# Kernel tuning notes

Measured on AMD Instinct MI355X. Metric: run time of the kernel, lower is better.

## Reference

```python
import jax, jax.numpy as jnp
import numpy as np
from jax import lax

EPS = 1e-5

def ste_sign(x):
    # forward-only module: plain sign is fine
    return jnp.sign(x)

def conv2d(x, w, pad):
    # x: NCHW, w: OIHW, stride 1
    return lax.conv_general_dilated(x, w, window_strides=(1, 1),
                                    padding=[(pad, pad), (pad, pad)],
                                    dimension_numbers=('NCHW', 'OIHW', 'NCHW'))

def maxpool2(x):
    # 2x2 max pool, stride 2, VALID (floor) -- matches nn.MaxPool2d(2,2)
    return lax.reduce_window(x, -jnp.inf, lax.max, (1, 1, 2, 2), (1, 1, 2, 2), 'VALID')

def batchnorm(x, gamma, beta):
    # training-mode BN: batch statistics over (N,H,W), biased variance
    mean = jnp.mean(x, axis=(0, 2, 3), keepdims=True)
    var = jnp.var(x, axis=(0, 2, 3), keepdims=True)
    xn = (x - mean) * lax.rsqrt(var + EPS)
    return xn * gamma[None, :, None, None] + beta[None, :, None, None]

def setup_inputs() -> dict:
    key = jax.random.key(0)
    ks = jax.random.split(key, 8)
    def he(k, shape):
        n = shape[2] * shape[3] * shape[0]
        return jax.random.normal(k, shape, jnp.float32) * np.sqrt(2.0 / n)
    x = jax.random.normal(ks[0], (4096, 1, 28, 28), jnp.float32)
    w0 = he(ks[1], (32, 1, 3, 3))
    w1 = he(ks[2], (32, 32, 3, 3))
    w2 = he(ks[3], (32, 32, 3, 3))
    g0 = jnp.ones((32,), jnp.float32); b0 = jnp.zeros((32,), jnp.float32)
    g1 = jnp.ones((32,), jnp.float32); b1 = jnp.zeros((32,), jnp.float32)
    g2 = jnp.ones((32,), jnp.float32); b2 = jnp.zeros((32,), jnp.float32)
    fw = jax.random.normal(ks[4], (10, 288), jnp.float32) * 0.01
    fb = jnp.zeros((10,), jnp.float32)
    return {"x": x, "w0": w0, "g0": g0, "b0": b0, "w1": w1, "g1": g1, "b1": b1,
            "w2": w2, "g2": g2, "b2": b2, "fw": fw, "fb": fb}

def reference(x, w0, g0, b0, w1, g1, b1, w2, g2, b2, fw, fb):
    # block0: fp conv -> pool -> bn (no act)
    h = batchnorm(maxpool2(conv2d(x, w0, 1)), g0, b0)          # [B,32,14,14]
    # block1: binary(1w1a) conv -> pool -> bn + maxpool(shortcut)
    o = batchnorm(maxpool2(conv2d(ste_sign(h), ste_sign(w1), 1)), g1, b1)
    h = o + maxpool2(h)                                         # [B,32,7,7]
    # block2
    o = batchnorm(maxpool2(conv2d(ste_sign(h), ste_sign(w2), 1)), g2, b2)
    h = o + maxpool2(h)                                         # [B,32,3,3]
    h = h.reshape(h.shape[0], -1)                                # [B,288]
    return h @ fw.T + fb                                         # [B,10]
```

## Files before the change

kernel.cpp:

```cpp
#include <hip/hip_runtime.h>
#include <stdint.h>

#define BATCH 4096

typedef float v16f __attribute__((ext_vector_type(16)));
typedef short v8s  __attribute__((ext_vector_type(8)));

__device__ __forceinline__ int sgn8(float v) {
    return (v > 0.f) ? 1 : ((v < 0.f) ? -1 : 0);
}

__global__ void k_signw1(const float* __restrict__ w, uint16_t* __restrict__ o) {
    int i = blockIdx.x * 256 + threadIdx.x;
    if (i >= 9216) return;
    int j = i & 7, n = (i >> 3) & 31, q = (i >> 8) & 1, kh = (i >> 9) & 1, tp = i >> 10;
    int cin = kh * 16 + q * 8 + j;
    float v = w[(n * 32 + cin) * 9 + tp];
    o[i] = (v > 0.f) ? 0x3F80 : ((v < 0.f) ? 0xBF80 : 0);
}

__global__ __launch_bounds__(448) void k_conv0(const float* __restrict__ x,
                                               const float* __restrict__ w0,
                                               float* __restrict__ p0,
                                               double* __restrict__ part0) {
    __shared__ float xs[960];
    __shared__ float wl[288];
    __shared__ double rs[32][14], rq[32][14];
    int n = blockIdx.x, t = threadIdx.x;
    for (int i = t; i < 960; i += 448) xs[i] = 0.f;
    for (int i = t; i < 288; i += 448) wl[i] = w0[i];
    __syncthreads();
    for (int i = t; i < 784; i += 448) {
        int y = i / 28, xx = i - y * 28;
        xs[(y + 1) * 32 + xx + 1] = x[n * 784 + i];
    }
    __syncthreads();
    int c = t & 31, py = t >> 5;
    float wreg[9];
    #pragma unroll
    for (int i = 0; i < 9; ++i) wreg[i] = wl[c * 9 + i];
    const float4* X4 = (const float4*)xs;
    float4 cur0 = X4[(2 * py + 0) * 8];
    float4 cur1 = X4[(2 * py + 1) * 8];
    float4 cur2 = X4[(2 * py + 2) * 8];
    float4 cur3 = X4[(2 * py + 3) * 8];
    double s = 0.0, q = 0.0;
    float* obase = p0 + ((size_t)n * 196 + py * 14) * 32 + c;
    #pragma unroll
    for (int k = 0; k < 7; ++k) {
        float4 n0 = X4[(2 * py + 0) * 8 + k + 1];
        float4 n1 = X4[(2 * py + 1) * 8 + k + 1];
        float4 n2 = X4[(2 * py + 2) * 8 + k + 1];
        float4 n3 = X4[(2 * py + 3) * 8 + k + 1];
        float a[4][6];
        a[0][0] = cur0.x; a[0][1] = cur0.y; a[0][2] = cur0.z; a[0][3] = cur0.w; a[0][4] = n0.x; a[0][5] = n0.y;
        a[1][0] = cur1.x; a[1][1] = cur1.y; a[1][2] = cur1.z; a[1][3] = cur1.w; a[1][4] = n1.x; a[1][5] = n1.y;
        a[2][0] = cur2.x; a[2][1] = cur2.y; a[2][2] = cur2.z; a[2][3] = cur2.w; a[2][4] = n2.x; a[2][5] = n2.y;
        a[3][0] = cur3.x; a[3][1] = cur3.y; a[3][2] = cur3.z; a[3][3] = cur3.w; a[3][4] = n3.x; a[3][5] = n3.y;
        #pragma unroll
        for (int e = 0; e < 2; ++e) {
            int base = 2 * e;
            float s00 = 0.f, s01 = 0.f, s10 = 0.f, s11 = 0.f;
            #pragma unroll
            for (int ky = 0; ky < 3; ++ky)
            #pragma unroll
            for (int kx = 0; kx < 3; ++kx) {
                float w = wreg[ky * 3 + kx];
                s00 = fmaf(a[ky][base + kx], w, s00);
                s01 = fmaf(a[ky][base + kx + 1], w, s01);
                s10 = fmaf(a[ky + 1][base + kx], w, s10);
                s11 = fmaf(a[ky + 1][base + kx + 1], w, s11);
            }
            float m = fmaxf(fmaxf(s00, s01), fmaxf(s10, s11));
            obase[(2 * k + e) * 32] = m;
            double v = (double)m;
            s += v; q += v * v;
        }
        cur0 = n0; cur1 = n1; cur2 = n2; cur3 = n3;
    }
    rs[c][py] = s; rq[c][py] = q;
    __syncthreads();
    if (t < 32) {
        double S = 0.0, Q = 0.0;
        #pragma unroll
        for (int i = 0; i < 14; ++i) { S += rs[t][i]; Q += rq[t][i]; }
        part0[(size_t)t * 4096 + n] = S;
        part0[(size_t)32 * 4096 + (size_t)t * 4096 + n] = Q;
    }
}

__global__ __launch_bounds__(256) void k_finalize(const double* __restrict__ part, int G,
                                                  const float* __restrict__ g,
                                                  const float* __restrict__ b,
                                                  double inv_count, float* __restrict__ ss) {
    int c = blockIdx.x, t = threadIdx.x;
    double s = 0.0, q = 0.0;
    for (int i = t; i < G; i += 256) {
        s += part[(size_t)c * G + i];
        q += part[(size_t)32 * G + (size_t)c * G + i];
    }
    #pragma unroll
    for (int o = 32; o > 0; o >>= 1) { s += __shfl_down(s, o); q += __shfl_down(q, o); }
    __shared__ double rs[4], rq[4];
    int w = t >> 6, l = t & 63;
    if (l == 0) { rs[w] = s; rq[w] = q; }
    __syncthreads();
    if (t == 0) {
        s = rs[0] + rs[1] + rs[2] + rs[3];
        q = rq[0] + rq[1] + rq[2] + rq[3];
        double mean = s * inv_count;
        double var = q * inv_count - mean * mean;
        double sc = (double)g[c] / sqrt(var + 1e-5);
        ss[c] = (float)sc;
        ss[32 + c] = (float)((double)b[c] - mean * sc);
    }
}

__global__ __launch_bounds__(256) void k_bn0(const float* __restrict__ p0,
                                             const float* __restrict__ ss,
                                             int8_t* __restrict__ s0,
                                             float* __restrict__ hp0) {
    __shared__ float P[6468];
    __shared__ float SS[64];
    int n = blockIdx.x, t = threadIdx.x;
    if (t < 64) SS[t] = ss[t];
    __syncthreads();
    const float4* src4 = (const float4*)(p0 + (size_t)n * 6272);
    uint32_t* s0w = (uint32_t*)(s0 + (size_t)n * 6272);
    for (int i = t; i < 1568; i += 256) {
        int pix = i >> 3, cg = i & 7;
        float4 v = src4[i];
        int c0 = cg * 4;
        float h0 = fmaf(SS[c0],     v.x, SS[32 + c0]);
        float h1 = fmaf(SS[c0 + 1], v.y, SS[33 + c0]);
        float h2 = fmaf(SS[c0 + 2], v.z, SS[34 + c0]);
        float h3 = fmaf(SS[c0 + 3], v.w, SS[35 + c0]);
        uint32_t u = (uint32_t)(uint8_t)(int8_t)sgn8(h0)
                   | ((uint32_t)(uint8_t)(int8_t)sgn8(h1)) << 8
                   | ((uint32_t)(uint8_t)(int8_t)sgn8(h2)) << 16
                   | ((uint32_t)(uint8_t)(int8_t)sgn8(h3)) << 24;
        s0w[i] = u;
        float* Pp = &P[pix * 33 + c0];
        Pp[0] = h0; Pp[1] = h1; Pp[2] = h2; Pp[3] = h3;
    }
    __syncthreads();
    if (t < 196) {
        int pw = t >> 2, oct = t & 3;
        int py = pw / 7, px = pw - py * 7;
        int b00 = ((2 * py) * 14 + 2 * px) * 33;
        int b01 = b00 + 33;
        int b10 = b00 + 14 * 33;
        int b11 = b10 + 33;
        float out[8];
        #pragma unroll
        for (int k = 0; k < 8; ++k) {
            int c = oct * 8 + k;
            out[k] = fmaxf(fmaxf(P[b00 + c], P[b01 + c]),
                           fmaxf(P[b10 + c], P[b11 + c]));
        }
        float4* hd = (float4*)(hp0 + ((size_t)n * 49 + pw) * 32 + oct * 8);
        float4 h0; h0.x = out[0]; h0.y = out[1]; h0.z = out[2]; h0.w = out[3];
        float4 h1; h1.x = out[4]; h1.y = out[5]; h1.z = out[6]; h1.w = out[7];
        hd[0] = h0; hd[1] = h1;
    }
}

__global__ __launch_bounds__(256) void k_conv1m(const int8_t* __restrict__ s0,
                                                const uint16_t* __restrict__ w1f,
                                                float* __restrict__ p1,
                                                double* __restrict__ part1) {
    __shared__ uint32_t lds[16384];
    int t = threadIdx.x;
    int n0 = blockIdx.x * 4;
    if (t < 240) {
        int img = t / 60, e = t % 60;
        int yh, xh;
        if (e < 16)      { yh = 0;      xh = e; }
        else if (e < 32) { yh = 15;     xh = e - 16; }
        else if (e < 46) { yh = e - 31; xh = 0; }
        else             { yh = e - 45; xh = 15; }
        uint32_t* d = &lds[img * 4096 + (yh * 16 + xh) * 16];
        uint4 z; z.x = z.y = z.z = z.w = 0u;
        ((uint4*)d)[0] = z; ((uint4*)d)[1] = z; ((uint4*)d)[2] = z; ((uint4*)d)[3] = z;
    }
    int lane = t & 63, wv = t >> 6;
    int q = lane >> 5, ncol = lane & 31;
    v8s wfr[18];
    #pragma unroll
    for (int f = 0; f < 18; ++f)
        wfr[f] = *(const v8s*)(w1f + (f * 2 + q) * 256 + ncol * 8);
    for (int i = t; i < 6272; i += 256) {
        int img = i / 1568, r = i - img * 1568;
        int pimg = r >> 3, dp = r & 7;
        int iy = pimg / 14, ix = pimg - iy * 14;
        int p = (iy + 1) * 16 + ix + 1;
        uint32_t u = ((const uint32_t*)s0)[(size_t)(n0 + img) * 1568 + r];
        uint32_t b0 = u & 0xFF, b1 = (u >> 8) & 0xFF, b2 = (u >> 16) & 0xFF, b3 = u >> 24;
        uint32_t h0 = b0 ? (0x3F80u | ((b0 & 0x80u) << 8)) : 0u;
        uint32_t h1 = b1 ? (0x3F80u | ((b1 & 0x80u) << 8)) : 0u;
        uint32_t h2 = b2 ? (0x3F80u | ((b2 & 0x80u) << 8)) : 0u;
        uint32_t h3 = b3 ? (0x3F80u | ((b3 & 0x80u) << 8)) : 0u;
        int g = dp >> 1;
        int gs = g ^ (p & 3);
        int idx = img * 4096 + p * 16 + (gs << 2) + ((dp & 1) << 1);
        lds[idx] = h0 | (h1 << 16);
        lds[idx + 1] = h2 | (h3 << 16);
    }
    __syncthreads();
    int n = n0 + wv;
    int ibase = wv * 4096;
    int m = lane & 31;
    int quad = m & 3, pwl = m >> 2;
    int dy = quad >> 1, dx = quad & 1;
    double sAcc = 0.0, qAcc = 0.0;
    for (int tile = 0; tile < 7; ++tile) {
        int pw = tile * 8 + pwl;
        int pwc = min(pw, 48);
        int py = pwc / 7, px = pwc - py * 7;
        int pbase = (2 * py + dy) * 16 + 2 * px + dx;
        v16f acc;
        #pragma unroll
        for (int i = 0; i < 16; ++i) acc[i] = 0.f;
        #pragma unroll
        for (int tp = 0; tp < 9; ++tp) {
            int p = pbase + (tp / 3) * 16 + (tp % 3);
            int psw = p & 3;
            #pragma unroll
            for (int kh = 0; kh < 2; ++kh) {
                int g = kh * 2 + q;
                int idx = ibase + p * 16 + ((g ^ psw) << 2);
                v8s a = *(const v8s*)&lds[idx];
                acc = __builtin_amdgcn_mfma_f32_32x32x16_bf16(a, wfr[tp * 2 + kh], acc, 0, 0, 0);
            }
        }
        #pragma unroll
        for (int g4 = 0; g4 < 4; ++g4) {
            float mx = fmaxf(fmaxf(acc[4 * g4], acc[4 * g4 + 1]),
                             fmaxf(acc[4 * g4 + 2], acc[4 * g4 + 3]));
            int pwo = tile * 8 + 2 * g4 + q;
            if (pwo < 49) {
                p1[((size_t)n * 49 + pwo) * 32 + ncol] = mx;
                double v = (double)mx;
                sAcc += v; qAcc += v * v;
            }
        }
    }
    __syncthreads();
    double* red = (double*)lds;
    red[(wv * 2 + q) * 32 + ncol] = sAcc;
    red[256 + (wv * 2 + q) * 32 + ncol] = qAcc;
    __syncthreads();
    if (t < 32) {
        double S = 0.0, Q = 0.0;
        #pragma unroll
        for (int i = 0; i < 8; ++i) { S += red[i * 32 + t]; Q += red[256 + i * 32 + t]; }
        part1[(size_t)t * 1024 + blockIdx.x] = S;
        part1[(size_t)32 * 1024 + (size_t)t * 1024 + blockIdx.x] = Q;
    }
}

__global__ __launch_bounds__(256) void k_bn1(const float* __restrict__ p1,
                                             const float* __restrict__ hp0,
                                             const float* __restrict__ ss,
                                             uint32_t* __restrict__ s1,
                                             float* __restrict__ hp1) {
    __shared__ float H[1568];
    int n = blockIdx.x, t = threadIdx.x;
    const float* P = p1 + (size_t)n * 1568;
    const float* Hp = hp0 + (size_t)n * 1568;
    for (int i = t; i < 1568; i += 256) {
        int c = i & 31;
        H[i] = fmaf(ss[64 + c], P[i], ss[96 + c]) + Hp[i];
    }
    __syncthreads();
    if (t < 32) {
        int c = t;
        uint32_t* sp = s1 + (size_t)n * 416 + c * 13;
        for (int j = 0; j < 13; ++j) {
            uint32_t u = 0;
            #pragma unroll
            for (int k = 0; k < 4; ++k) {
                int f = 4 * j + k;
                int sv = (f < 49) ? sgn8(H[f * 32 + c]) : 0;
                u |= ((uint32_t)(uint8_t)(int8_t)sv) << (8 * k);
            }
            sp[j] = u;
        }
    }
    for (int jj = t; jj < 288; jj += 256) {
        int c = jj / 9, pix = jj - c * 9;
        int r = pix / 3, qq = pix - r * 3;
        float a0 = H[((2 * r) * 7 + 2 * qq) * 32 + c];
        float a1 = H[((2 * r) * 7 + 2 * qq + 1) * 32 + c];
        float a2 = H[((2 * r + 1) * 7 + 2 * qq) * 32 + c];
        float a3 = H[((2 * r + 1) * 7 + 2 * qq + 1) * 32 + c];
        hp1[n * 288 + c * 9 + pix] = fmaxf(fmaxf(a0, a1), fmaxf(a2, a3));
    }
}

__global__ __launch_bounds__(256) void k_conv2m(const uint32_t* __restrict__ s1,
                                                const uint16_t* __restrict__ w2f,
                                                float* __restrict__ p2,
                                                double* __restrict__ part2) {
    __shared__ uint32_t lds[8192];
    int t = threadIdx.x;
    int n0 = blockIdx.x * 8;
    for (int i = t; i < 120; i += 256) {
        int img = i / 15, e = i - img * 15;
        int p = (e < 8) ? e : (e - 7) * 8;
        uint32_t* d = &lds[img * 1024 + p * 16];
        uint4 z; z.x = z.y = z.z = z.w = 0u;
        ((uint4*)d)[0] = z; ((uint4*)d)[1] = z; ((uint4*)d)[2] = z; ((uint4*)d)[3] = z;
    }
    int lane = t & 63, wv = t >> 6;
    int q = lane >> 5, ncol = lane & 31;
    v8s wfr[18];
    #pragma unroll
    for (int f = 0; f < 18; ++f)
        wfr[f] = *(const v8s*)(w2f + (f * 2 + q) * 256 + ncol * 8);
    for (int i = t; i < 1664; i += 256) {
        int img = i / 208, r = i - img * 208;
        int c2 = r / 13, j = r - c2 * 13;
        const uint32_t* sb = s1 + (size_t)(n0 + img) * 416;
        uint32_t wa = sb[(2 * c2) * 13 + j];
        uint32_t wb = sb[(2 * c2 + 1) * 13 + j];
        int g = c2 >> 2, sub = c2 & 3;
        #pragma unroll
        for (int k = 0; k < 4; ++k) {
            int f = 4 * j + k;
            if (f < 49) {
                int y = f / 7, x = f - y * 7;
                int p = (y + 1) * 8 + (x + 1);
                uint32_t ba = (wa >> (8 * k)) & 0xFF;
                uint32_t bb = (wb >> (8 * k)) & 0xFF;
                uint32_t ha = ba ? (0x3F80u | ((ba & 0x80u) << 8)) : 0u;
                uint32_t hb = bb ? (0x3F80u | ((bb & 0x80u) << 8)) : 0u;
                lds[img * 1024 + p * 16 + ((g ^ (p & 3)) << 2) + sub] = ha | (hb << 16);
            }
        }
    }
    __syncthreads();
    int m = lane & 31;
    int quad = m & 3, pwl = m >> 2;
    int dy = quad >> 1, dx = quad & 1;
    double sAcc = 0.0, qAcc = 0.0;
    for (int tile = wv; tile < 9; tile += 4) {
        int pwg = tile * 8 + pwl;
        int img = pwg / 9, pwi = pwg - img * 9;
        int py = pwi / 3, px = pwi - py * 3;
        int pbase = (2 * py + dy) * 8 + 2 * px + dx;
        v16f acc;
        #pragma unroll
        for (int i = 0; i < 16; ++i) acc[i] = 0.f;
        #pragma unroll
        for (int tp = 0; tp < 9; ++tp) {
            int p = pbase + (tp / 3) * 8 + (tp % 3);
            int psw = p & 3;
            #pragma unroll
            for (int kh = 0; kh < 2; ++kh) {
                int g = kh * 2 + q;
                int idx = img * 1024 + p * 16 + ((g ^ psw) << 2);
                v8s a = *(const v8s*)&lds[idx];
                acc = __builtin_amdgcn_mfma_f32_32x32x16_bf16(a, wfr[tp * 2 + kh], acc, 0, 0, 0);
            }
        }
        #pragma unroll
        for (int g4 = 0; g4 < 4; ++g4) {
            float mx = fmaxf(fmaxf(acc[4 * g4], acc[4 * g4 + 1]),
                             fmaxf(acc[4 * g4 + 2], acc[4 * g4 + 3]));
            int pwo = tile * 8 + 2 * g4 + q;
            int oimg = pwo / 9, opwi = pwo - oimg * 9;
            p2[(size_t)(n0 + oimg) * 288 + ncol * 9 + opwi] = mx;
            double v = (double)mx;
            sAcc += v; qAcc += v * v;
        }
    }
    __syncthreads();
    double* red = (double*)lds;
    red[(wv * 2 + q) * 32 + ncol] = sAcc;
    red[256 + (wv * 2 + q) * 32 + ncol] = qAcc;
    __syncthreads();
    if (t < 32) {
        double S = 0.0, Q = 0.0;
        #pragma unroll
        for (int i = 0; i < 8; ++i) { S += red[i * 32 + t]; Q += red[256 + i * 32 + t]; }
        part2[(size_t)t * 512 + blockIdx.x] = S;
        part2[(size_t)32 * 512 + (size_t)t * 512 + blockIdx.x] = Q;
    }
}

__global__ __launch_bounds__(256) void k_fc(const float* __restrict__ p2,
                                            const float* __restrict__ hp1,
                                            const float* __restrict__ ss,
                                            const float* __restrict__ fw,
                                            const float* __restrict__ fb,
                                            float* __restrict__ outv) {
    int wv = threadIdx.x >> 6, l = threadIdx.x & 63;
    int n = blockIdx.x * 4 + wv;
    float acc[10];
    #pragma unroll
    for (int k = 0; k < 10; ++k) acc[k] = 0.f;
    #pragma unroll
    for (int i = 0; i < 5; ++i) {
        int j = l + 64 * i;
        if (j < 288) {
            int c = j / 9;
            float h = fmaf(ss[128 + c], p2[n * 288 + j], ss[160 + c]) + hp1[n * 288 + j];
            #pragma unroll
            for (int k = 0; k < 10; ++k)
                acc[k] = fmaf(h, fw[k * 288 + j], acc[k]);
        }
    }
    #pragma unroll
    for (int k = 0; k < 10; ++k) {
        float s = acc[k];
        #pragma unroll
        for (int o = 32; o > 0; o >>= 1) s += __shfl_down(s, o);
        if (l == 0) outv[n * 10 + k] = s + fb[k];
    }
}

extern "C" void kernel_launch(void* const* d_in, const int* in_sizes, int n_in,
                              void* d_out, int out_size, void* d_ws, size_t ws_size,
                              hipStream_t stream) {
    (void)in_sizes; (void)n_in; (void)out_size; (void)ws_size;
    const float* x  = (const float*)d_in[0];
    const float* w0 = (const float*)d_in[1];
    const float* g0 = (const float*)d_in[2];
    const float* b0 = (const float*)d_in[3];
    const float* w1 = (const float*)d_in[4];
    const float* g1 = (const float*)d_in[5];
    const float* b1 = (const float*)d_in[6];
    const float* w2 = (const float*)d_in[7];
    const float* g2 = (const float*)d_in[8];
    const float* b2 = (const float*)d_in[9];
    const float* fw = (const float*)d_in[10];
    const float* fb = (const float*)d_in[11];
    float* outv = (float*)d_out;
    char* ws = (char*)d_ws;

    float*     ss    = (float*)(ws + 1024);
    uint16_t*  w1f   = (uint16_t*)(ws + 2048);
    uint16_t*  w2f   = (uint16_t*)(ws + 38912);
    float*     p0    = (float*)(ws + 76800);
    float*     p1    = (float*)(ws + 76800);
    uint32_t*  s1    = (uint32_t*)(ws + 25766912);
    float*     hp1   = (float*)(ws + 32582656);
    float*     p2    = (float*)(ws + 37301248);
    double*    part1 = (double*)(ws + 60000000);
    int8_t*    s0    = (int8_t*)(ws + 102837248);
    double*    part0 = (double*)(ws + 102837248);
    double*    part2 = (double*)(ws + 102837248);
    float*     hp0   = (float*)(ws + 128527360);

    k_signw1<<<36, 256, 0, stream>>>(w1, w1f);
    k_signw1<<<36, 256, 0, stream>>>(w2, w2f);

    k_conv0<<<BATCH, 448, 0, stream>>>(x, w0, p0, part0);
    k_finalize<<<32, 256, 0, stream>>>(part0, 4096, g0, b0, 1.0 / (BATCH * 196.0), ss);
    k_bn0<<<BATCH, 256, 0, stream>>>(p0, ss, s0, hp0);

    k_conv1m<<<BATCH / 4, 256, 0, stream>>>(s0, w1f, p1, part1);
    k_finalize<<<32, 256, 0, stream>>>(part1, 1024, g1, b1, 1.0 / (BATCH * 49.0), ss + 64);
    k_bn1<<<BATCH, 256, 0, stream>>>(p1, hp0, ss, s1, hp1);

    k_conv2m<<<BATCH / 8, 256, 0, stream>>>(s1, w2f, p2, part2);
    k_finalize<<<32, 256, 0, stream>>>(part2, 512, g2, b2, 1.0 / (BATCH * 9.0), ss + 128);

    k_fc<<<BATCH / 4, 256, 0, stream>>>(p2, hp1, ss, fw, fb, outv);
}
```

Before: 223.0 us.

## Recompute conv0 in BN0 pass and emit padded swizzled bf16 sign tiles

The first conv no longer writes its pooled fp32 output to global memory; it only produces batch statistics. A new BN0 kernel recomputes the cheap 1-channel conv, applies BN in registers, and writes the sign activations directly as a padded, XOR-swizzled bf16 layout that conv1 can bulk-copy into LDS without decoding. Conv1 now handles 2 images per block with two waves per image, so its grid and the partial-stat count double. This trades a second pass of conv0 arithmetic for removing the p0 round trip and conv1's int8-to-bf16 unpack, but the bf16 sign tensor (16 KB per image) is larger than the old int8 one.

```diff
diff --git a/kernel.cpp b/kernel.cpp
--- a/kernel.cpp
+++ b/kernel.cpp
@@ -19,10 +19,9 @@
     o[i] = (v > 0.f) ? 0x3F80 : ((v < 0.f) ? 0xBF80 : 0);
 }
 
-__global__ __launch_bounds__(448) void k_conv0(const float* __restrict__ x,
-                                               const float* __restrict__ w0,
-                                               float* __restrict__ p0,
-                                               double* __restrict__ part0) {
+__global__ __launch_bounds__(448) void k_conv0s(const float* __restrict__ x,
+                                                const float* __restrict__ w0,
+                                                double* __restrict__ part0) {
     __shared__ float xs[960];
     __shared__ float wl[288];
     __shared__ double rs[32][14], rq[32][14];
@@ -45,7 +44,6 @@
     float4 cur2 = X4[(2 * py + 2) * 8];
     float4 cur3 = X4[(2 * py + 3) * 8];
     double s = 0.0, q = 0.0;
-    float* obase = p0 + ((size_t)n * 196 + py * 14) * 32 + c;
     #pragma unroll
     for (int k = 0; k < 7; ++k) {
         float4 n0 = X4[(2 * py + 0) * 8 + k + 1];
@@ -72,7 +70,6 @@
                 s11 = fmaf(a[ky + 1][base + kx + 1], w, s11);
             }
             float m = fmaxf(fmaxf(s00, s01), fmaxf(s10, s11));
-            obase[(2 * k + e) * 32] = m;
             double v = (double)m;
             s += v; q += v * v;
         }
@@ -116,104 +113,141 @@
     }
 }
 
-__global__ __launch_bounds__(256) void k_bn0(const float* __restrict__ p0,
-                                             const float* __restrict__ ss,
-                                             int8_t* __restrict__ s0,
-                                             float* __restrict__ hp0) {
+__global__ __launch_bounds__(448) void k_bn0r(const float* __restrict__ x,
+                                              const float* __restrict__ w0,
+                                              const float* __restrict__ ss,
+                                              uint32_t* __restrict__ s0b,
+                                              float* __restrict__ hp0) {
+    __shared__ float xs[960];
+    __shared__ float wl[288];
     __shared__ float P[6468];
-    __shared__ float SS[64];
     int n = blockIdx.x, t = threadIdx.x;
-    if (t < 64) SS[t] = ss[t];
-    __syncthreads();
-    const float4* src4 = (const float4*)(p0 + (size_t)n * 6272);
-    uint32_t* s0w = (uint32_t*)(s0 + (size_t)n * 6272);
-    for (int i = t; i < 1568; i += 256) {
-        int pix = i >> 3, cg = i & 7;
-        float4 v = src4[i];
-        int c0 = cg * 4;
-        float h0 = fmaf(SS[c0],     v.x, SS[32 + c0]);
-        float h1 = fmaf(SS[c0 + 1], v.y, SS[33 + c0]);
-        float h2 = fmaf(SS[c0 + 2], v.z, SS[34 + c0]);
-        float h3 = fmaf(SS[c0 + 3], v.w, SS[35 + c0]);
-        uint32_t u = (uint32_t)(uint8_t)(int8_t)sgn8(h0)
-                   | ((uint32_t)(uint8_t)(int8_t)sgn8(h1)) << 8
-                   | ((uint32_t)(uint8_t)(int8_t)sgn8(h2)) << 16
-                   | ((uint32_t)(uint8_t)(int8_t)sgn8(h3)) << 24;
-        s0w[i] = u;
-        float* Pp = &P[pix * 33 + c0];
-        Pp[0] = h0; Pp[1] = h1; Pp[2] = h2; Pp[3] = h3;
-    }
-    __syncthreads();
-    if (t < 196) {
-        int pw = t >> 2, oct = t & 3;
-        int py = pw / 7, px = pw - py * 7;
-        int b00 = ((2 * py) * 14 + 2 * px) * 33;
-        int b01 = b00 + 33;
-        int b10 = b00 + 14 * 33;
-        int b11 = b10 + 33;
-        float out[8];
-        #pragma unroll
-        for (int k = 0; k < 8; ++k) {
-            int c = oct * 8 + k;
-            out[k] = fmaxf(fmaxf(P[b00 + c], P[b01 + c]),
-                           fmaxf(P[b10 + c], P[b11 + c]));
-        }
-        float4* hd = (float4*)(hp0 + ((size_t)n * 49 + pw) * 32 + oct * 8);
-        float4 h0; h0.x = out[0]; h0.y = out[1]; h0.z = out[2]; h0.w = out[3];
-        float4 h1; h1.x = out[4]; h1.y = out[5]; h1.z = out[6]; h1.w = out[7];
-        hd[0] = h0; hd[1] = h1;
-    }
-}
-
-__global__ __launch_bounds__(256) void k_conv1m(const int8_t* __restrict__ s0,
-                                                const uint16_t* __restrict__ w1f,
-                                                float* __restrict__ p1,
-                                                double* __restrict__ part1) {
-    __shared__ uint32_t lds[16384];
-    int t = threadIdx.x;
-    int n0 = blockIdx.x * 4;
+    for (int i = t; i < 960; i += 448) xs[i] = 0.f;
+    for (int i = t; i < 288; i += 448) wl[i] = w0[i];
+    __syncthreads();
+    for (int i = t; i < 784; i += 448) {
+        int y = i / 28, xx = i - y * 28;
+        xs[(y + 1) * 32 + xx + 1] = x[n * 784 + i];
+    }
+    __syncthreads();
+    int c = t & 31, py = t >> 5;
+    float wreg[9];
+    #pragma unroll
+    for (int i = 0; i < 9; ++i) wreg[i] = wl[c * 9 + i];
+    float sc = ss[c], sh = ss[32 + c];
+    const float4* X4 = (const float4*)xs;
+    float4 cur0 = X4[(2 * py + 0) * 8];
+    float4 cur1 = X4[(2 * py + 1) * 8];
+    float4 cur2 = X4[(2 * py + 2) * 8];
+    float4 cur3 = X4[(2 * py + 3) * 8];
+    #pragma unroll
+    for (int k = 0; k < 7; ++k) {
+        float4 n0 = X4[(2 * py + 0) * 8 + k + 1];
+        float4 n1 = X4[(2 * py + 1) * 8 + k + 1];
+        float4 n2 = X4[(2 * py + 2) * 8 + k + 1];
+        float4 n3 = X4[(2 * py + 3) * 8 + k + 1];
+        float a[4][6];
+        a[0][0] = cur0.x; a[0][1] = cur0.y; a[0][2] = cur0.z; a[0][3] = cur0.w; a[0][4] = n0.x; a[0][5] = n0.y;
+        a[1][0] = cur1.x; a[1][1] = cur1.y; a[1][2] = cur1.z; a[1][3] = cur1.w; a[1][4] = n1.x; a[1][5] = n1.y;
+        a[2][0] = cur2.x; a[2][1] = cur2.y; a[2][2] = cur2.z; a[2][3] = cur2.w; a[2][4] = n2.x; a[2][5] = n2.y;
+        a[3][0] = cur3.x; a[3][1] = cur3.y; a[3][2] = cur3.z; a[3][3] = cur3.w; a[3][4] = n3.x; a[3][5] = n3.y;
+        #pragma unroll
+        for (int e = 0; e < 2; ++e) {
+            int base = 2 * e;
+            float s00 = 0.f, s01 = 0.f, s10 = 0.f, s11 = 0.f;
+            #pragma unroll
+            for (int ky = 0; ky < 3; ++ky)
+            #pragma unroll
+            for (int kx = 0; kx < 3; ++kx) {
+                float w = wreg[ky * 3 + kx];
+                s00 = fmaf(a[ky][base + kx], w, s00);
+                s01 = fmaf(a[ky][base + kx + 1], w, s01);
+                s10 = fmaf(a[ky + 1][base + kx], w, s10);
+                s11 = fmaf(a[ky + 1][base + kx + 1], w, s11);
+            }
+            float m = fmaxf(fmaxf(s00, s01), fmaxf(s10, s11));
+            P[(py * 14 + 2 * k + e) * 33 + c] = fmaf(sc, m, sh);
+        }
+        cur0 = n0; cur1 = n1; cur2 = n2; cur3 = n3;
+    }
+    __syncthreads();
+    uint32_t* simg = s0b + (size_t)n * 4096;
+    for (int i = t; i < 784; i += 448) {
+        int pl = i >> 2, qd = i & 3;
+        int iy = pl / 14, ix = pl - iy * 14;
+        int yy = iy + 1, xx2 = ix + 1;
+        int p = yy * 16 + xx2;
+        int psw = (xx2 & 3) ^ (yy & 3);
+        int g = qd ^ psw;
+        const float* Pp = &P[pl * 33 + g * 8];
+        uint32_t d[4];
+        #pragma unroll
+        for (int j = 0; j < 4; ++j) {
+            float h0 = Pp[2 * j], h1 = Pp[2 * j + 1];
+            uint32_t b0 = (h0 > 0.f) ? 0x3F80u : ((h0 < 0.f) ? 0xBF80u : 0u);
+            uint32_t b1 = (h1 > 0.f) ? 0x3F80u : ((h1 < 0.f) ? 0xBF80u : 0u);
+            d[j] = b0 | (b1 << 16);
+        }
+        uint4 v; v.x = d[0]; v.y = d[1]; v.z = d[2]; v.w = d[3];
+        *(uint4*)(simg + p * 16 + qd * 4) = v;
+    }
     if (t < 240) {
-        int img = t / 60, e = t % 60;
+        int e = t >> 2, qd = t & 3;
         int yh, xh;
         if (e < 16)      { yh = 0;      xh = e; }
         else if (e < 32) { yh = 15;     xh = e - 16; }
         else if (e < 46) { yh = e - 31; xh = 0; }
         else             { yh = e - 45; xh = 15; }
-        uint32_t* d = &lds[img * 4096 + (yh * 16 + xh) * 16];
         uint4 z; z.x = z.y = z.z = z.w = 0u;
-        ((uint4*)d)[0] = z; ((uint4*)d)[1] = z; ((uint4*)d)[2] = z; ((uint4*)d)[3] = z;
-    }
+        *(uint4*)(simg + (yh * 16 + xh) * 16 + qd * 4) = z;
+    }
+    if (t < 196) {
+        int pw = t >> 2, oct = t & 3;
+        int pyy = pw / 7, pxx = pw - pyy * 7;
+        int b00 = ((2 * pyy) * 14 + 2 * pxx) * 33;
+        int b01 = b00 + 33;
+        int b10 = b00 + 14 * 33;
+        int b11 = b10 + 33;
+        float out[8];
+        #pragma unroll
+        for (int k = 0; k < 8; ++k) {
+            int cc = oct * 8 + k;
+            out[k] = fmaxf(fmaxf(P[b00 + cc], P[b01 + cc]),
+                           fmaxf(P[b10 + cc], P[b11 + cc]));
+        }
+        float4* hd = (float4*)(hp0 + ((size_t)n * 49 + pw) * 32 + oct * 8);
+        float4 h0; h0.x = out[0]; h0.y = out[1]; h0.z = out[2]; h0.w = out[3];
+        float4 h1; h1.x = out[4]; h1.y = out[5]; h1.z = out[6]; h1.w = out[7];
+        hd[0] = h0; hd[1] = h1;
+    }
+}
+
+__global__ __launch_bounds__(256) void k_conv1m(const uint32_t* __restrict__ s0b,
+                                                const uint16_t* __restrict__ w1f,
+                                                float* __restrict__ p1,
+                                                double* __restrict__ part1) {
+    __shared__ uint32_t lds[8192];
+    int t = threadIdx.x;
+    int n0 = blockIdx.x * 2;
+    const uint4* gp = (const uint4*)(s0b + (size_t)n0 * 4096);
+    uint4* lp = (uint4*)lds;
+    #pragma unroll
+    for (int i = 0; i < 8; ++i) lp[t + i * 256] = gp[t + i * 256];
     int lane = t & 63, wv = t >> 6;
     int q = lane >> 5, ncol = lane & 31;
     v8s wfr[18];
     #pragma unroll
     for (int f = 0; f < 18; ++f)
         wfr[f] = *(const v8s*)(w1f + (f * 2 + q) * 256 + ncol * 8);
-    for (int i = t; i < 6272; i += 256) {
-        int img = i / 1568, r = i - img * 1568;
-        int pimg = r >> 3, dp = r & 7;
-        int iy = pimg / 14, ix = pimg - iy * 14;
-        int p = (iy + 1) * 16 + ix + 1;
-        uint32_t u = ((const uint32_t*)s0)[(size_t)(n0 + img) * 1568 + r];
-        uint32_t b0 = u & 0xFF, b1 = (u >> 8) & 0xFF, b2 = (u >> 16) & 0xFF, b3 = u >> 24;
-        uint32_t h0 = b0 ? (0x3F80u | ((b0 & 0x80u) << 8)) : 0u;
-        uint32_t h1 = b1 ? (0x3F80u | ((b1 & 0x80u) << 8)) : 0u;
-        uint32_t h2 = b2 ? (0x3F80u | ((b2 & 0x80u) << 8)) : 0u;
-        uint32_t h3 = b3 ? (0x3F80u | ((b3 & 0x80u) << 8)) : 0u;
-        int g = dp >> 1;
-        int gs = g ^ (p & 3);
-        int idx = img * 4096 + p * 16 + (gs << 2) + ((dp & 1) << 1);
-        lds[idx] = h0 | (h1 << 16);
-        lds[idx + 1] = h2 | (h3 << 16);
-    }
-    __syncthreads();
-    int n = n0 + wv;
-    int ibase = wv * 4096;
+    __syncthreads();
+    int img = wv >> 1, wh = wv & 1;
+    int n = n0 + img;
+    int ibase = img * 4096;
     int m = lane & 31;
     int quad = m & 3, pwl = m >> 2;
     int dy = quad >> 1, dx = quad & 1;
     double sAcc = 0.0, qAcc = 0.0;
-    for (int tile = 0; tile < 7; ++tile) {
+    for (int tile = wh; tile < 7; tile += 2) {
         int pw = tile * 8 + pwl;
         int pwc = min(pw, 48);
         int py = pwc / 7, px = pwc - py * 7;
@@ -224,7 +258,7 @@
         #pragma unroll
         for (int tp = 0; tp < 9; ++tp) {
             int p = pbase + (tp / 3) * 16 + (tp % 3);
-            int psw = p & 3;
+            int psw = (p ^ (p >> 4)) & 3;
             #pragma unroll
             for (int kh = 0; kh < 2; ++kh) {
                 int g = kh * 2 + q;
@@ -254,8 +288,8 @@
         double S = 0.0, Q = 0.0;
         #pragma unroll
         for (int i = 0; i < 8; ++i) { S += red[i * 32 + t]; Q += red[256 + i * 32 + t]; }
-        part1[(size_t)t * 1024 + blockIdx.x] = S;
-        part1[(size_t)32 * 1024 + (size_t)t * 1024 + blockIdx.x] = Q;
+        part1[(size_t)t * 2048 + blockIdx.x] = S;
+        part1[(size_t)32 * 2048 + (size_t)t * 2048 + blockIdx.x] = Q;
     }
 }
 
@@ -442,26 +476,25 @@
     float*     ss    = (float*)(ws + 1024);
     uint16_t*  w1f   = (uint16_t*)(ws + 2048);
     uint16_t*  w2f   = (uint16_t*)(ws + 38912);
-    float*     p0    = (float*)(ws + 76800);
     float*     p1    = (float*)(ws + 76800);
     uint32_t*  s1    = (uint32_t*)(ws + 25766912);
     float*     hp1   = (float*)(ws + 32582656);
     float*     p2    = (float*)(ws + 37301248);
-    double*    part1 = (double*)(ws + 60000000);
-    int8_t*    s0    = (int8_t*)(ws + 102837248);
-    double*    part0 = (double*)(ws + 102837248);
-    double*    part2 = (double*)(ws + 102837248);
+    uint32_t*  s0b   = (uint32_t*)(ws + 42019840);
+    double*    part0 = (double*)(ws + 109128704);
+    double*    part1 = (double*)(ws + 111225856);
+    double*    part2 = (double*)(ws + 112274432);
     float*     hp0   = (float*)(ws + 128527360);
 
     k_signw1<<<36, 256, 0, stream>>>(w1, w1f);
     k_signw1<<<36, 256, 0, stream>>>(w2, w2f);
 
-    k_conv0<<<BATCH, 448, 0, stream>>>(x, w0, p0, part0);
+    k_conv0s<<<BATCH, 448, 0, stream>>>(x, w0, part0);
     k_finalize<<<32, 256, 0, stream>>>(part0, 4096, g0, b0, 1.0 / (BATCH * 196.0), ss);
-    k_bn0<<<BATCH, 256, 0, stream>>>(p0, ss, s0, hp0);
-
-    k_conv1m<<<BATCH / 4, 256, 0, stream>>>(s0, w1f, p1, part1);
-    k_finalize<<<32, 256, 0, stream>>>(part1, 1024, g1, b1, 1.0 / (BATCH * 49.0), ss + 64);
+    k_bn0r<<<BATCH, 448, 0, stream>>>(x, w0, ss, s0b, hp0);
+
+    k_conv1m<<<BATCH / 2, 256, 0, stream>>>(s0b, w1f, p1, part1);
+    k_finalize<<<32, 256, 0, stream>>>(part1, 2048, g1, b1, 1.0 / (BATCH * 49.0), ss + 64);
     k_bn1<<<BATCH, 256, 0, stream>>>(p1, hp0, ss, s1, hp1);
 
     k_conv2m<<<BATCH / 8, 256, 0, stream>>>(s1, w2f, p2, part2);
```

Measured after the change: 217.9 us. 1.02x faster.
